# Kernel tuning notes

Hardware: AMD Instinct MI355X
Metric: run time of the kernel (lower is better)

The kernel has to match this reference:

```python
import jax, jax.numpy as jnp
import numpy as np

TAU = 0.5

def setup_inputs() -> dict:
    key = jax.random.key(0)
    ks = jax.random.split(key, 6)
    B, L, D, P = 4, 4096, 256, 256
    return {
        "X1": jax.random.normal(ks[0], (B, L, D), dtype=jnp.float32),
        "X2": jax.random.normal(ks[1], (B, L, D), dtype=jnp.float32),
        "W1": jax.random.normal(ks[2], (P, D), dtype=jnp.float32) * (1.0 / np.sqrt(D)),
        "b1": jax.random.normal(ks[3], (P,), dtype=jnp.float32) * 0.01,
        "W2": jax.random.normal(ks[4], (D, P), dtype=jnp.float32) * (1.0 / np.sqrt(P)),
        "b2": jax.random.normal(ks[5], (D,), dtype=jnp.float32) * 0.01,
    }

def _projection(z, W1, b1, W2, b2):
    h = jax.nn.elu(z @ W1.T + b1)
    return h @ W2.T + b2

def _normalize(z, eps=1e-12):
    n = jnp.linalg.norm(z, axis=-1, keepdims=True)
    return z / jnp.maximum(n, eps)

def _semi_loss(z1, z2, tau):
    # z1, z2: [B, L, D]
    z1n = _normalize(z1)
    z2n = _normalize(z2)
    refl = jnp.exp(jnp.einsum('bld,bmd->blm', z1n, z1n) / tau)   # [B, L, L]
    between = jnp.exp(jnp.einsum('bld,bmd->blm', z1n, z2n) / tau)
    refl_diag = jnp.diagonal(refl, axis1=-2, axis2=-1)           # [B, L]
    between_diag = jnp.diagonal(between, axis1=-2, axis2=-1)
    denom = refl.sum(axis=-1) + between.sum(axis=-1) - refl_diag
    return -jnp.log(between_diag / denom).sum(axis=-1)           # [B]

def reference(X1, X2, W1, b1, W2, b2):
    h1 = _projection(X1, W1, b1, W2, b2)
    h2 = _projection(X2, W1, b1, W2, b2)
    l1 = _semi_loss(h1, h2, TAU)
    l2 = _semi_loss(h2, h1, TAU)
    return ((l1 + l2) * 0.5).mean()
```

## Files before the change

### kernel.cpp

```cpp
#include <hip/hip_runtime.h>
#include <math.h>


typedef __attribute__((ext_vector_type(8))) short short8;
typedef __attribute__((ext_vector_type(4))) short short4v;
typedef __attribute__((ext_vector_type(4))) float float4v;
typedef __attribute__((ext_vector_type(8))) int int8v;
typedef __attribute__((ext_vector_type(4))) int int4v;

#if defined(__has_builtin)
#if __has_builtin(__builtin_amdgcn_exp2f)
#define EXP2F(x) __builtin_amdgcn_exp2f(x)
#endif
#endif
#ifndef EXP2F
#define EXP2F(x) __expf(0.69314718056f * (x))
#endif

__device__ __forceinline__ short f2bf(float f) {
    unsigned u = __builtin_bit_cast(unsigned, f);
    u += 0x7fffu + ((u >> 16) & 1u);
    return (short)(u >> 16);
}

__device__ __forceinline__ unsigned char f2fp8(float f) {
    float af = fabsf(f);
    unsigned s = (__builtin_bit_cast(unsigned, f) >> 31) << 7;
    if (af < 0.015625f) {
        int q = (int)rintf(af * 512.0f);
        return (unsigned char)(s | (unsigned)q);
    }
    unsigned au = __builtin_bit_cast(unsigned, af);
    au += 0x7FFFFu + ((au >> 20) & 1u);
    int e = (int)(au >> 23) - 127;
    unsigned m = (au >> 20) & 7u;
    return (unsigned char)(s | (unsigned)((e + 7) << 3) | m);
}

__device__ __forceinline__ void gl_lds16(const void* g, void* l) {
    __builtin_amdgcn_global_load_lds(
        (const __attribute__((address_space(1))) void*)g,
        (__attribute__((address_space(3))) void*)l, 16, 0, 0);
}

__device__ __forceinline__ void gemm256_core(
    const short* __restrict__ A, const short* __restrict__ B,
    int arow0, short* lsA, short* lsB, float4v acc[4][4])
{
    const int tid  = threadIdx.x;
    const int w    = tid >> 6;
    const int lane = tid & 63;
    const int l15  = lane & 15;

    for (int kt = 0; kt < 4; ++kt) {
        const int kbase = kt * 64;
#pragma unroll
        for (int r = 0; r < 10; ++r) {
            const int c = w * 10 + r;
            if (c < 8) {
                const int s   = c * 64 + lane;
                const int kc  = s >> 6;
                const int row = s & 63;
                gl_lds16(A + (size_t)(arow0 + row) * 256 + kbase + kc * 8,
                         lsA + (size_t)c * 512);
            } else {
                const int s   = (c - 8) * 64 + lane;
                const int kc  = s >> 8;
                const int row = s & 255;
                gl_lds16(B + (size_t)row * 256 + kbase + kc * 8,
                         lsB + (size_t)(c - 8) * 512);
            }
        }
        __syncthreads();
#pragma unroll
        for (int ks = 0; ks < 2; ++ks) {
            const int kc = ks * 4 + (lane >> 4);
            short8 af[4], bfv[4];
#pragma unroll
            for (int mi = 0; mi < 4; ++mi)
                af[mi] = *(const short8*)(lsA + ((size_t)kc * 64 + mi * 16 + l15) * 8);
#pragma unroll
            for (int ni = 0; ni < 4; ++ni)
                bfv[ni] = *(const short8*)(lsB + ((size_t)kc * 256 + w * 64 + ni * 16 + l15) * 8);
#pragma unroll
            for (int mi = 0; mi < 4; ++mi)
#pragma unroll
                for (int ni = 0; ni < 4; ++ni)
                    acc[mi][ni] = __builtin_amdgcn_mfma_f32_16x16x32_bf16(
                        af[mi], bfv[ni], acc[mi][ni], 0, 0, 0);
        }
        __syncthreads();
    }
}

__global__ __launch_bounds__(256) void convX_kernel(
    const float* __restrict__ X1, const float* __restrict__ X2,
    short* __restrict__ dst)
{
    int i = blockIdx.x * 256 + threadIdx.x;
    const float* src = (i < 1048576) ? X1 : X2;
    int j = i & 1048575;
    float4v v = ((const float4v*)src)[j];
    short4v o;
    o.x = f2bf(v.x); o.y = f2bf(v.y); o.z = f2bf(v.z); o.w = f2bf(v.w);
    ((short4v*)dst)[i] = o;
}

__global__ __launch_bounds__(256) void convW_kernel(
    const float* __restrict__ W1, const float* __restrict__ W2,
    short* __restrict__ d1, short* __restrict__ d2)
{
    int i = blockIdx.x * 256 + threadIdx.x;
    const float* src = (i < 16384) ? W1 : W2;
    short* dst = (i < 16384) ? d1 : d2;
    int j = i & 16383;
    float4v v = ((const float4v*)src)[j];
    short4v o;
    o.x = f2bf(v.x); o.y = f2bf(v.y); o.z = f2bf(v.z); o.w = f2bf(v.w);
    ((short4v*)dst)[j] = o;
}

__global__ __launch_bounds__(256, 2) void fusedproj_kernel(
    const short* __restrict__ Xbf, const short* __restrict__ W1bf,
    const float* __restrict__ b1, const short* __restrict__ W2bf,
    const float* __restrict__ b2, unsigned char* __restrict__ zn8)
{
    __shared__ short lsA[4096];
    __shared__ short lsB[16384];
    __shared__ short lsH[16384];
    __shared__ float rssq[4][64];
    __shared__ float rinv[64];

    const int arow0 = blockIdx.x * 64;
    const int tid  = threadIdx.x;
    const int w    = tid >> 6;
    const int lane = tid & 63;
    const int quad = lane >> 4;
    const int l15  = lane & 15;

    float4v acc[4][4];
#pragma unroll
    for (int mi = 0; mi < 4; ++mi)
#pragma unroll
        for (int ni = 0; ni < 4; ++ni)
            acc[mi][ni] = (float4v){0.f, 0.f, 0.f, 0.f};

    gemm256_core(Xbf, W1bf, arow0, lsA, lsB, acc);

    {
        const int rowbase = quad * 4;
        const int colbase = w * 64 + l15;
#pragma unroll
        for (int ni = 0; ni < 4; ++ni) {
            const int p  = colbase + ni * 16;
            const float bv = b1[p];
#pragma unroll
            for (int mi = 0; mi < 4; ++mi)
#pragma unroll
                for (int reg = 0; reg < 4; ++reg) {
                    const int row = rowbase + mi * 16 + reg;
                    float v = acc[mi][ni][reg] + bv;
                    v = (v > 0.f) ? v : expm1f(v);
                    lsH[(size_t)(p >> 3) * 512 + row * 8 + (p & 7)] = f2bf(v);
                }
        }
    }

#pragma unroll
    for (int mi = 0; mi < 4; ++mi)
#pragma unroll
        for (int ni = 0; ni < 4; ++ni)
            acc[mi][ni] = (float4v){0.f, 0.f, 0.f, 0.f};

    for (int kt = 0; kt < 4; ++kt) {
        const int kbase = kt * 64;
#pragma unroll
        for (int r = 0; r < 8; ++r) {
            const int c   = w * 8 + r;
            const int s   = c * 64 + lane;
            const int kc  = s >> 8;
            const int row = s & 255;
            gl_lds16(W2bf + (size_t)row * 256 + kbase + kc * 8,
                     lsB + (size_t)c * 512);
        }
        __syncthreads();
#pragma unroll
        for (int ks = 0; ks < 2; ++ks) {
            const int kc = ks * 4 + quad;
            short8 af[4], bfv[4];
#pragma unroll
            for (int mi = 0; mi < 4; ++mi)
                af[mi] = *(const short8*)(lsH +
                    ((size_t)(kt * 8 + kc) * 64 + mi * 16 + l15) * 8);
#pragma unroll
            for (int ni = 0; ni < 4; ++ni)
                bfv[ni] = *(const short8*)(lsB +
                    ((size_t)kc * 256 + w * 64 + ni * 16 + l15) * 8);
#pragma unroll
            for (int mi = 0; mi < 4; ++mi)
#pragma unroll
                for (int ni = 0; ni < 4; ++ni)
                    acc[mi][ni] = __builtin_amdgcn_mfma_f32_16x16x32_bf16(
                        af[mi], bfv[ni], acc[mi][ni], 0, 0, 0);
        }
        __syncthreads();
    }

#pragma unroll
    for (int ni = 0; ni < 4; ++ni) {
        const float bv = b2[w * 64 + ni * 16 + l15];
#pragma unroll
        for (int mi = 0; mi < 4; ++mi)
#pragma unroll
            for (int reg = 0; reg < 4; ++reg)
                acc[mi][ni][reg] += bv;
    }
    float ps[4][4];
#pragma unroll
    for (int mi = 0; mi < 4; ++mi)
#pragma unroll
        for (int reg = 0; reg < 4; ++reg) {
            float s = 0.f;
#pragma unroll
            for (int ni = 0; ni < 4; ++ni) {
                float v = acc[mi][ni][reg];
                s += v * v;
            }
            s += __shfl_xor(s, 1); s += __shfl_xor(s, 2);
            s += __shfl_xor(s, 4); s += __shfl_xor(s, 8);
            ps[mi][reg] = s;
        }
    if (l15 == 0) {
#pragma unroll
        for (int mi = 0; mi < 4; ++mi)
#pragma unroll
            for (int reg = 0; reg < 4; ++reg)
                rssq[w][mi * 16 + quad * 4 + reg] = ps[mi][reg];
    }
    __syncthreads();
    if (tid < 64) {
        float ssq = rssq[0][tid] + rssq[1][tid] + rssq[2][tid] + rssq[3][tid];
        rinv[tid] = 1.69864360f / fmaxf(sqrtf(ssq), 1e-12f);
    }
    __syncthreads();

    const int r0  = arow0;
    const int set = r0 >> 14;
    const int bb  = (r0 >> 12) & 3;
    const int l0  = r0 & 4095;
    unsigned char* dst = zn8 + ((size_t)(bb * 2 + set) * 4096 + l0) * 256;
    const int colbase = w * 64 + l15;
#pragma unroll
    for (int mi = 0; mi < 4; ++mi)
#pragma unroll
        for (int reg = 0; reg < 4; ++reg) {
            const int rl = mi * 16 + quad * 4 + reg;
            const float inv = rinv[rl];
#pragma unroll
            for (int ni = 0; ni < 4; ++ni)
                dst[(size_t)rl * 256 + colbase + ni * 16] =
                    f2fp8(acc[mi][ni][reg] * inv);
        }
}

#if defined(__has_builtin)
#if __has_builtin(__builtin_amdgcn_mfma_scale_f32_16x16x128_f8f6f4)
#define HAVE_MX 1
#endif
#endif

__global__ __launch_bounds__(256, 2) void gram_fp8_sym_kernel(
    const unsigned char* __restrict__ zn8, float* __restrict__ S,
    float* __restrict__ Cc, float* __restrict__ out)
{
    __shared__ unsigned char lsB[2][32768];

    const int bx    = blockIdx.x;
    const int xcd   = bx & 7;
    const int batch = xcd >> 1;
    const int sub   = (bx >> 3) * 2 + (xcd & 1);
    const int p     = sub >> 2;
    const int qu    = sub & 3;
    const int u0    = (qu == 0) ? 0 : 17 + (qu - 1) * 16;
    const int u1    = u0 + ((qu == 0) ? 17 : 16);
    const int ubrk  = 64 - p;

    const unsigned char* Z = zn8 + (size_t)batch * 2097152;

    const int tid  = threadIdx.x;
    const int w    = tid >> 6;
    const int lane = tid & 63;
    const int wm   = w & 1;
    const int wn   = w >> 1;
    const int quad = lane >> 4;
    const int l15  = lane & 15;

#define TJ_OF(u)  ((u) < ubrk ? p + (u) : (u) - 1)
#define ROW_OF(u) ((u) < ubrk ? p : 63 - p)

#define STAGE_B(t, buf)                                                       \
    {                                                                         \
        const unsigned char* Bb = Z + (size_t)(t) * 128 * 256;                \
        _Pragma("unroll")                                                     \
        for (int r = 0; r < 8; ++r) {                                         \
            const int c   = w * 8 + r;                                        \
            const int u_  = c * 64 + lane;                                    \
            const int kp  = u_ >> 7;                                          \
            const int col = u_ & 127;                                         \
            gl_lds16(Bb + (size_t)col * 256 + kp * 16,                        \
                     &lsB[buf][(size_t)c * 1024]);                            \
        }                                                                     \
    }

    float rs[4][4];
#pragma unroll
    for (int mi = 0; mi < 4; ++mi)
#pragma unroll
        for (int reg = 0; reg < 4; ++reg)
            rs[mi][reg] = 0.f;
    float dsum = 0.f;

#define FLUSH_RS(rowstripe)                                                   \
    {                                                                         \
        float* Sr = S + (size_t)batch * 8192 + (rowstripe) * 128 + wm * 64;   \
        _Pragma("unroll")                                                     \
        for (int mi = 0; mi < 4; ++mi)                                        \
            _Pragma("unroll")                                                 \
            for (int reg = 0; reg < 4; ++reg) {                               \
                float v = rs[mi][reg];                                        \
                v += __shfl_xor(v, 1); v += __shfl_xor(v, 2);                 \
                v += __shfl_xor(v, 4); v += __shfl_xor(v, 8);                 \
                if (l15 == 0)                                                 \
                    atomicAdd(&Sr[mi * 16 + quad * 4 + reg], v);              \
                rs[mi][reg] = 0.f;                                            \
            }                                                                 \
    }

    int currow = ROW_OF(u0);

#ifdef HAVE_MX
    int8v afr[4][2];
#define LOAD_A(rowstripe)                                                     \
    {                                                                         \
        const unsigned char* Ab = Z + (size_t)((rowstripe) * 128 + wm * 64) * 256; \
        _Pragma("unroll")                                                     \
        for (int mi = 0; mi < 4; ++mi)                                        \
            _Pragma("unroll")                                                 \
            for (int ks = 0; ks < 2; ++ks) {                                  \
                const unsigned char* pA = Ab + (size_t)(mi * 16 + l15) * 256  \
                                          + ks * 128 + quad * 32;             \
                int4v lo = *(const int4v*)pA;                                 \
                int4v hi = *(const int4v*)(pA + 16);                          \
                afr[mi][ks] = __builtin_shufflevector(lo, hi, 0,1,2,3,4,5,6,7); \
            }                                                                 \
    }
#else
    long afr[4][8];
#define LOAD_A(rowstripe)                                                     \
    {                                                                         \
        const unsigned char* Ab = Z + (size_t)((rowstripe) * 128 + wm * 64) * 256; \
        _Pragma("unroll")                                                     \
        for (int mi = 0; mi < 4; ++mi)                                        \
            _Pragma("unroll")                                                 \
            for (int kc = 0; kc < 8; ++kc)                                    \
                afr[mi][kc] = *(const long*)(Ab + (size_t)(mi * 16 + l15) * 256 \
                                             + kc * 32 + quad * 8);           \
    }
#endif

    LOAD_A(currow);
    STAGE_B(TJ_OF(u0), 0);
    __syncthreads();

    for (int ui = u0; ui < u1; ++ui) {
        const int buf = (ui - u0) & 1;
        const int row = ROW_OF(ui);
        const int tj  = TJ_OF(ui);
        if (row != currow) {
            FLUSH_RS(currow);
            LOAD_A(row);
            currow = row;
        }
        if (ui + 1 < u1) STAGE_B(TJ_OF(ui + 1), buf ^ 1);

        float4v acc[4][4];
#pragma unroll
        for (int mi = 0; mi < 4; ++mi)
#pragma unroll
            for (int ni = 0; ni < 4; ++ni)
                acc[mi][ni] = (float4v){0.f, 0.f, 0.f, 0.f};

        const unsigned char* lb = &lsB[buf][0];
        __builtin_amdgcn_s_setprio(1);
#ifdef HAVE_MX
#pragma unroll
        for (int ks = 0; ks < 2; ++ks) {
            const int kp0 = ks * 8 + quad * 2;
            int8v bfv[4];
#pragma unroll
            for (int ni = 0; ni < 4; ++ni) {
                const unsigned char* pB = lb +
                    ((size_t)kp0 * 128 + wn * 64 + ni * 16 + l15) * 16;
                int4v lo = *(const int4v*)pB;
                int4v hi = *(const int4v*)(pB + 2048);
                bfv[ni] = __builtin_shufflevector(lo, hi, 0,1,2,3,4,5,6,7);
            }
#pragma unroll
            for (int mi = 0; mi < 4; ++mi)
#pragma unroll
                for (int ni = 0; ni < 4; ++ni)
                    acc[mi][ni] = __builtin_amdgcn_mfma_scale_f32_16x16x128_f8f6f4(
                        afr[mi][ks], bfv[ni], acc[mi][ni],
                        0, 0,
                        0, 0x7F7F7F7F,
                        0, 0x7F7F7F7F);
        }
#else
#pragma unroll
        for (int kc = 0; kc < 8; ++kc) {
            const int kseg = kc * 4 + quad;
            const int kp   = kseg >> 1;
            const int hf   = kseg & 1;
            long bfv[4];
#pragma unroll
            for (int ni = 0; ni < 4; ++ni)
                bfv[ni] = *(const long*)(lb +
                    ((size_t)kp * 128 + wn * 64 + ni * 16 + l15) * 16 + hf * 8);
#pragma unroll
            for (int mi = 0; mi < 4; ++mi)
#pragma unroll
                for (int ni = 0; ni < 4; ++ni)
                    acc[mi][ni] = __builtin_amdgcn_mfma_f32_16x16x32_fp8_fp8(
                        afr[mi][kc], bfv[ni], acc[mi][ni], 0, 0, 0);
        }
#endif
        __builtin_amdgcn_s_setprio(0);

        if (tj == row + 32) {
#pragma unroll
            for (int mi = 0; mi < 4; ++mi)
#pragma unroll
                for (int ni = 0; ni < 4; ++ni)
#pragma unroll
                    for (int reg = 0; reg < 4; ++reg) {
                        const int r = wm * 64 + mi * 16 + quad * 4 + reg;
                        const int c = wn * 64 + ni * 16 + l15;
                        if (r == c) dsum += acc[mi][ni][reg];
                    }
        }

#pragma unroll
        for (int mi = 0; mi < 4; ++mi)
#pragma unroll
            for (int ni = 0; ni < 4; ++ni)
#pragma unroll
                for (int reg = 0; reg < 4; ++reg)
                    acc[mi][ni][reg] = EXP2F(acc[mi][ni][reg]);

#pragma unroll
        for (int mi = 0; mi < 4; ++mi)
#pragma unroll
            for (int reg = 0; reg < 4; ++reg)
                rs[mi][reg] += acc[mi][0][reg] + acc[mi][1][reg]
                             + acc[mi][2][reg] + acc[mi][3][reg];

        if (tj > row) {
            float* Cd = Cc + ((size_t)batch * 128 + row * 2 + wm) * 8192
                        + tj * 128 + wn * 64;
#pragma unroll
            for (int ni = 0; ni < 4; ++ni) {
                float s = 0.f;
#pragma unroll
                for (int mi = 0; mi < 4; ++mi)
#pragma unroll
                    for (int reg = 0; reg < 4; ++reg)
                        s += acc[mi][ni][reg];
                s += __shfl_xor(s, 16); s += __shfl_xor(s, 32);
                if (quad == 0)
                    Cd[ni * 16 + l15] = s;
            }
        }
        __syncthreads();
    }

    FLUSH_RS(currow);

    {
        float dv = dsum;
        dv += __shfl_xor(dv, 1);  dv += __shfl_xor(dv, 2);
        dv += __shfl_xor(dv, 4);  dv += __shfl_xor(dv, 8);
        dv += __shfl_xor(dv, 16); dv += __shfl_xor(dv, 32);
        if (lane == 0 && dv != 0.f)
            atomicAdd(out, -0.17328680f * dv);
    }
#undef STAGE_B
#undef LOAD_A
#undef FLUSH_RS
#undef TJ_OF
#undef ROW_OF
}

__global__ __launch_bounds__(256) void final_log_kernel(
    const float* __restrict__ S, const float* __restrict__ Cc,
    float* __restrict__ out)
{
    __shared__ float red[4];
    const int tid  = threadIdx.x;
    const int w    = tid >> 6;
    const int lane = tid & 63;
    const float E2 = 7.3890560989306495f;

    const int i = blockIdx.x * 256 + tid;
    const int b = i >> 13;
    const int q = i & 8191;
    float s = S[i];
    const float* Cp = Cc + (size_t)b * 128 * 8192 + q;
    const int np = (q >> 7) * 2;
    for (int r = 0; r < np; ++r)
        s += Cp[(size_t)r * 8192];
    float acc = logf(s - E2);

    acc += __shfl_xor(acc, 1);  acc += __shfl_xor(acc, 2);
    acc += __shfl_xor(acc, 4);  acc += __shfl_xor(acc, 8);
    acc += __shfl_xor(acc, 16); acc += __shfl_xor(acc, 32);
    if (lane == 0) red[w] = acc;
    __syncthreads();
    if (tid == 0)
        atomicAdd(out, 0.125f * (red[0] + red[1] + red[2] + red[3]));
}

extern "C" void kernel_launch(void* const* d_in, const int* in_sizes, int n_in,
                              void* d_out, int out_size, void* d_ws, size_t ws_size,
                              hipStream_t stream)
{
    const float* X1 = (const float*)d_in[0];
    const float* X2 = (const float*)d_in[1];
    const float* W1 = (const float*)d_in[2];
    const float* b1 = (const float*)d_in[3];
    const float* W2 = (const float*)d_in[4];
    const float* b2 = (const float*)d_in[5];

    char* ws = (char*)d_ws;
    float* S    = (float*)(ws + 0);
    short* W1bf = (short*)(ws + 131072);
    short* W2bf = (short*)(ws + 262144);
    short* Xbf  = (short*)(ws + 393216);
    float* Cc   = (float*)(ws + 393216);
    unsigned char* zn8 = (unsigned char*)(ws + 17170432);

    hipMemsetAsync(S, 0, 131072, stream);
    hipMemsetAsync(d_out, 0, sizeof(float), stream);

    convW_kernel<<<128, 256, 0, stream>>>(W1, W2, W1bf, W2bf);
    convX_kernel<<<8192, 256, 0, stream>>>(X1, X2, Xbf);
    fusedproj_kernel<<<512, 256, 0, stream>>>(Xbf, W1bf, b1, W2bf, b2, zn8);
    gram_fp8_sym_kernel<<<512, 256, 0, stream>>>(zn8, S, Cc, (float*)d_out);
    final_log_kernel<<<128, 256, 0, stream>>>(S, Cc, (float*)d_out);
}
```

Baseline: 213.7 us.

## Fuse X conversion into projection, fold memsets, drop LDS staging in gram

Removes the separate convX kernel: the projection kernel now reads fp32 X directly from global memory and converts to bf16 in registers for its A fragments. Folds the S and output zeroing into the weight conversion kernel, replacing two memset calls. The gram kernel no longer double-buffers B tiles through LDS; it loads fp8 B fragments straight from global memory and drops the per-iteration barrier. This saves launches and an intermediate bf16 round trip, but adds uncoalesced global reads and loses LDS reuse in both GEMMs.

```diff
diff --git a/kernel.cpp b/kernel.cpp
--- a/kernel.cpp
+++ b/kernel.cpp
@@ -43,72 +43,10 @@
         (__attribute__((address_space(3))) void*)l, 16, 0, 0);
 }
 
-__device__ __forceinline__ void gemm256_core(
-    const short* __restrict__ A, const short* __restrict__ B,
-    int arow0, short* lsA, short* lsB, float4v acc[4][4])
-{
-    const int tid  = threadIdx.x;
-    const int w    = tid >> 6;
-    const int lane = tid & 63;
-    const int l15  = lane & 15;
-
-    for (int kt = 0; kt < 4; ++kt) {
-        const int kbase = kt * 64;
-#pragma unroll
-        for (int r = 0; r < 10; ++r) {
-            const int c = w * 10 + r;
-            if (c < 8) {
-                const int s   = c * 64 + lane;
-                const int kc  = s >> 6;
-                const int row = s & 63;
-                gl_lds16(A + (size_t)(arow0 + row) * 256 + kbase + kc * 8,
-                         lsA + (size_t)c * 512);
-            } else {
-                const int s   = (c - 8) * 64 + lane;
-                const int kc  = s >> 8;
-                const int row = s & 255;
-                gl_lds16(B + (size_t)row * 256 + kbase + kc * 8,
-                         lsB + (size_t)(c - 8) * 512);
-            }
-        }
-        __syncthreads();
-#pragma unroll
-        for (int ks = 0; ks < 2; ++ks) {
-            const int kc = ks * 4 + (lane >> 4);
-            short8 af[4], bfv[4];
-#pragma unroll
-            for (int mi = 0; mi < 4; ++mi)
-                af[mi] = *(const short8*)(lsA + ((size_t)kc * 64 + mi * 16 + l15) * 8);
-#pragma unroll
-            for (int ni = 0; ni < 4; ++ni)
-                bfv[ni] = *(const short8*)(lsB + ((size_t)kc * 256 + w * 64 + ni * 16 + l15) * 8);
-#pragma unroll
-            for (int mi = 0; mi < 4; ++mi)
-#pragma unroll
-                for (int ni = 0; ni < 4; ++ni)
-                    acc[mi][ni] = __builtin_amdgcn_mfma_f32_16x16x32_bf16(
-                        af[mi], bfv[ni], acc[mi][ni], 0, 0, 0);
-        }
-        __syncthreads();
-    }
-}
-
-__global__ __launch_bounds__(256) void convX_kernel(
-    const float* __restrict__ X1, const float* __restrict__ X2,
-    short* __restrict__ dst)
-{
-    int i = blockIdx.x * 256 + threadIdx.x;
-    const float* src = (i < 1048576) ? X1 : X2;
-    int j = i & 1048575;
-    float4v v = ((const float4v*)src)[j];
-    short4v o;
-    o.x = f2bf(v.x); o.y = f2bf(v.y); o.z = f2bf(v.z); o.w = f2bf(v.w);
-    ((short4v*)dst)[i] = o;
-}
-
-__global__ __launch_bounds__(256) void convW_kernel(
+__global__ __launch_bounds__(256) void convW_zero_kernel(
     const float* __restrict__ W1, const float* __restrict__ W2,
-    short* __restrict__ d1, short* __restrict__ d2)
+    short* __restrict__ d1, short* __restrict__ d2,
+    float* __restrict__ S, float* __restrict__ out)
 {
     int i = blockIdx.x * 256 + threadIdx.x;
     const float* src = (i < 16384) ? W1 : W2;
@@ -118,14 +56,16 @@
     short4v o;
     o.x = f2bf(v.x); o.y = f2bf(v.y); o.z = f2bf(v.z); o.w = f2bf(v.w);
     ((short4v*)dst)[j] = o;
+    S[i] = 0.f;
+    if (i == 0) *out = 0.f;
 }
 
 __global__ __launch_bounds__(256, 2) void fusedproj_kernel(
-    const short* __restrict__ Xbf, const short* __restrict__ W1bf,
-    const float* __restrict__ b1, const short* __restrict__ W2bf,
-    const float* __restrict__ b2, unsigned char* __restrict__ zn8)
+    const float* __restrict__ X1, const float* __restrict__ X2,
+    const short* __restrict__ W1bf, const float* __restrict__ b1,
+    const short* __restrict__ W2bf, const float* __restrict__ b2,
+    unsigned char* __restrict__ zn8)
 {
-    __shared__ short lsA[4096];
     __shared__ short lsB[16384];
     __shared__ short lsH[16384];
     __shared__ float rssq[4][64];
@@ -138,6 +78,9 @@
     const int quad = lane >> 4;
     const int l15  = lane & 15;
 
+    const int set = arow0 >> 14;
+    const float* Xs = (set ? X2 : X1) + (size_t)(arow0 & 16383) * 256;
+
     float4v acc[4][4];
 #pragma unroll
     for (int mi = 0; mi < 4; ++mi)
@@ -145,7 +88,48 @@
         for (int ni = 0; ni < 4; ++ni)
             acc[mi][ni] = (float4v){0.f, 0.f, 0.f, 0.f};
 
-    gemm256_core(Xbf, W1bf, arow0, lsA, lsB, acc);
+    for (int kt = 0; kt < 4; ++kt) {
+        const int kbase = kt * 64;
+#pragma unroll
+        for (int r = 0; r < 8; ++r) {
+            const int c   = w * 8 + r;
+            const int s   = c * 64 + lane;
+            const int kc  = s >> 8;
+            const int row = s & 255;
+            gl_lds16(W1bf + (size_t)row * 256 + kbase + kc * 8,
+                     lsB + (size_t)c * 512);
+        }
+        __syncthreads();
+#pragma unroll
+        for (int ks = 0; ks < 2; ++ks) {
+            const int kc = ks * 4 + quad;
+            short8 af[4], bfv[4];
+#pragma unroll
+            for (int mi = 0; mi < 4; ++mi) {
+                const float* xp = Xs + (size_t)(mi * 16 + l15) * 256
+                                  + kbase + kc * 8;
+                float4v a0 = *(const float4v*)xp;
+                float4v a1 = *(const float4v*)(xp + 4);
+                short8 t;
+                t[0] = f2bf(a0.x); t[1] = f2bf(a0.y);
+                t[2] = f2bf(a0.z); t[3] = f2bf(a0.w);
+                t[4] = f2bf(a1.x); t[5] = f2bf(a1.y);
+                t[6] = f2bf(a1.z); t[7] = f2bf(a1.w);
+                af[mi] = t;
+            }
+#pragma unroll
+            for (int ni = 0; ni < 4; ++ni)
+                bfv[ni] = *(const short8*)(lsB +
+                    ((size_t)kc * 256 + w * 64 + ni * 16 + l15) * 8);
+#pragma unroll
+            for (int mi = 0; mi < 4; ++mi)
+#pragma unroll
+                for (int ni = 0; ni < 4; ++ni)
+                    acc[mi][ni] = __builtin_amdgcn_mfma_f32_16x16x32_bf16(
+                        af[mi], bfv[ni], acc[mi][ni], 0, 0, 0);
+        }
+        __syncthreads();
+    }
 
     {
         const int rowbase = quad * 4;
@@ -245,7 +229,6 @@
     __syncthreads();
 
     const int r0  = arow0;
-    const int set = r0 >> 14;
     const int bb  = (r0 >> 12) & 3;
     const int l0  = r0 & 4095;
     unsigned char* dst = zn8 + ((size_t)(bb * 2 + set) * 4096 + l0) * 256;
@@ -273,8 +256,6 @@
     const unsigned char* __restrict__ zn8, float* __restrict__ S,
     float* __restrict__ Cc, float* __restrict__ out)
 {
-    __shared__ unsigned char lsB[2][32768];
-
     const int bx    = blockIdx.x;
     const int xcd   = bx & 7;
     const int batch = xcd >> 1;
@@ -297,20 +278,6 @@
 
 #define TJ_OF(u)  ((u) < ubrk ? p + (u) : (u) - 1)
 #define ROW_OF(u) ((u) < ubrk ? p : 63 - p)
-
-#define STAGE_B(t, buf)                                                       \
-    {                                                                         \
-        const unsigned char* Bb = Z + (size_t)(t) * 128 * 256;                \
-        _Pragma("unroll")                                                     \
-        for (int r = 0; r < 8; ++r) {                                         \
-            const int c   = w * 8 + r;                                        \
-            const int u_  = c * 64 + lane;                                    \
-            const int kp  = u_ >> 7;                                          \
-            const int col = u_ & 127;                                         \
-            gl_lds16(Bb + (size_t)col * 256 + kp * 16,                        \
-                     &lsB[buf][(size_t)c * 1024]);                            \
-        }                                                                     \
-    }
 
     float rs[4][4];
 #pragma unroll
@@ -369,11 +336,8 @@
 #endif
 
     LOAD_A(currow);
-    STAGE_B(TJ_OF(u0), 0);
-    __syncthreads();
 
     for (int ui = u0; ui < u1; ++ui) {
-        const int buf = (ui - u0) & 1;
         const int row = ROW_OF(ui);
         const int tj  = TJ_OF(ui);
         if (row != currow) {
@@ -381,7 +345,8 @@
             LOAD_A(row);
             currow = row;
         }
-        if (ui + 1 < u1) STAGE_B(TJ_OF(ui + 1), buf ^ 1);
+
+        const unsigned char* Bb = Z + ((size_t)tj * 128 + wn * 64) * 256;
 
         float4v acc[4][4];
 #pragma unroll
@@ -390,42 +355,39 @@
             for (int ni = 0; ni < 4; ++ni)
                 acc[mi][ni] = (float4v){0.f, 0.f, 0.f, 0.f};
 
-        const unsigned char* lb = &lsB[buf][0];
+#ifdef HAVE_MX
+        int8v bfv[2][4];
+#pragma unroll
+        for (int ks = 0; ks < 2; ++ks)
+#pragma unroll
+            for (int ni = 0; ni < 4; ++ni) {
+                const unsigned char* pB = Bb + (size_t)(ni * 16 + l15) * 256
+                                          + ks * 128 + quad * 32;
+                int4v lo = *(const int4v*)pB;
+                int4v hi = *(const int4v*)(pB + 16);
+                bfv[ks][ni] = __builtin_shufflevector(lo, hi, 0,1,2,3,4,5,6,7);
+            }
         __builtin_amdgcn_s_setprio(1);
-#ifdef HAVE_MX
-#pragma unroll
-        for (int ks = 0; ks < 2; ++ks) {
-            const int kp0 = ks * 8 + quad * 2;
-            int8v bfv[4];
-#pragma unroll
-            for (int ni = 0; ni < 4; ++ni) {
-                const unsigned char* pB = lb +
-                    ((size_t)kp0 * 128 + wn * 64 + ni * 16 + l15) * 16;
-                int4v lo = *(const int4v*)pB;
-                int4v hi = *(const int4v*)(pB + 2048);
-                bfv[ni] = __builtin_shufflevector(lo, hi, 0,1,2,3,4,5,6,7);
-            }
+#pragma unroll
+        for (int ks = 0; ks < 2; ++ks)
 #pragma unroll
             for (int mi = 0; mi < 4; ++mi)
 #pragma unroll
                 for (int ni = 0; ni < 4; ++ni)
                     acc[mi][ni] = __builtin_amdgcn_mfma_scale_f32_16x16x128_f8f6f4(
-                        afr[mi][ks], bfv[ni], acc[mi][ni],
+                        afr[mi][ks], bfv[ks][ni], acc[mi][ni],
                         0, 0,
                         0, 0x7F7F7F7F,
                         0, 0x7F7F7F7F);
-        }
+        __builtin_amdgcn_s_setprio(0);
 #else
 #pragma unroll
         for (int kc = 0; kc < 8; ++kc) {
-            const int kseg = kc * 4 + quad;
-            const int kp   = kseg >> 1;
-            const int hf   = kseg & 1;
             long bfv[4];
 #pragma unroll
             for (int ni = 0; ni < 4; ++ni)
-                bfv[ni] = *(const long*)(lb +
-                    ((size_t)kp * 128 + wn * 64 + ni * 16 + l15) * 16 + hf * 8);
+                bfv[ni] = *(const long*)(Bb + (size_t)(ni * 16 + l15) * 256
+                                         + kc * 32 + quad * 8);
 #pragma unroll
             for (int mi = 0; mi < 4; ++mi)
 #pragma unroll
@@ -434,7 +396,6 @@
                         afr[mi][kc], bfv[ni], acc[mi][ni], 0, 0, 0);
         }
 #endif
-        __builtin_amdgcn_s_setprio(0);
 
         if (tj == row + 32) {
 #pragma unroll
@@ -480,7 +441,6 @@
                     Cd[ni * 16 + l15] = s;
             }
         }
-        __syncthreads();
     }
 
     FLUSH_RS(currow);
@@ -493,7 +453,6 @@
         if (lane == 0 && dv != 0.f)
             atomicAdd(out, -0.17328680f * dv);
     }
-#undef STAGE_B
 #undef LOAD_A
 #undef FLUSH_RS
 #undef TJ_OF
@@ -544,16 +503,12 @@
     float* S    = (float*)(ws + 0);
     short* W1bf = (short*)(ws + 131072);
     short* W2bf = (short*)(ws + 262144);
-    short* Xbf  = (short*)(ws + 393216);
-    float* Cc   = (float*)(ws + 393216);
-    unsigned char* zn8 = (unsigned char*)(ws + 17170432);
-
-    hipMemsetAsync(S, 0, 131072, stream);
-    hipMemsetAsync(d_out, 0, sizeof(float), stream);
-
-    convW_kernel<<<128, 256, 0, stream>>>(W1, W2, W1bf, W2bf);
-    convX_kernel<<<8192, 256, 0, stream>>>(X1, X2, Xbf);
-    fusedproj_kernel<<<512, 256, 0, stream>>>(Xbf, W1bf, b1, W2bf, b2, zn8);
+    unsigned char* zn8 = (unsigned char*)(ws + 393216);
+    float* Cc   = (float*)(ws + 8781824);
+
+    convW_zero_kernel<<<128, 256, 0, stream>>>(W1, W2, W1bf, W2bf,
+                                               S, (float*)d_out);
+    fusedproj_kernel<<<512, 256, 0, stream>>>(X1, X2, W1bf, b1, W2bf, b2, zn8);
     gram_fp8_sym_kernel<<<512, 256, 0, stream>>>(zn8, S, Cc, (float*)d_out);
     final_log_kernel<<<128, 256, 0, stream>>>(S, Cc, (float*)d_out);
 }
```

After: 223.0 us. 4.3% more time.
